# Kernel optimization log

Hardware: AMD Instinct MI355X
Metric: run time of the kernel (lower is better)

Reference implementation:

```python
import jax, jax.numpy as jnp
import numpy as np

B, D, H, W, C = 2, 16, 56, 56, 128
WD, WH, WW = 2, 7, 7
SD, SH, SW = 1, 3, 3
HEADS = 4
HEAD_DIM = C // HEADS
N = WD * WH * WW            # tokens per window = 98
NW = (D // WD) * (H // WH) * (W // WW)  # windows per batch = 512
EPS = 1e-5
SCALE = HEAD_DIM ** -0.5


def _partition_np(x):
    b, d, h, w, c = x.shape
    x = x.reshape(b, d // WD, WD, h // WH, WH, w // WW, WW, c)
    return x.transpose(0, 1, 3, 5, 2, 4, 6, 7).reshape(-1, N, c)


def _compute_attn_mask():
    # cyclic-shift mask: label 3x3x3 regions, windows mix labels -> -100
    img = np.zeros((1, D, H, W, 1), np.float32)
    cnt = 0
    for ds in (slice(0, -WD), slice(-WD, -SD), slice(-SD, None)):
        for hs in (slice(0, -WH), slice(-WH, -SH), slice(-SH, None)):
            for ws in (slice(0, -WW), slice(-WW, -SW), slice(-SW, None)):
                img[:, ds, hs, ws, :] = cnt
                cnt += 1
    mw = _partition_np(img).reshape(-1, N)          # (nW, N)
    am = mw[:, None, :] - mw[:, :, None]
    return np.where(am != 0, -100.0, 0.0).astype(np.float32)


def _rel_index():
    coords = np.stack(np.meshgrid(np.arange(WD), np.arange(WH), np.arange(WW), indexing='ij')).reshape(3, -1)
    rel = (coords[:, :, None] - coords[:, None, :]).transpose(1, 2, 0)  # (N,N,3)
    rel[..., 0] += WD - 1
    rel[..., 1] += WH - 1
    rel[..., 2] += WW - 1
    rel[..., 0] *= (2 * WH - 1) * (2 * WW - 1)
    rel[..., 1] *= 2 * WW - 1
    return rel.sum(-1).astype(np.int32)  # (N,N)


def setup_inputs() -> dict:
    key = jax.random.key(0)
    ks = jax.random.split(key, 8)
    s = 0.02
    table_size = (2 * WD - 1) * (2 * WH - 1) * (2 * WW - 1)
    return {
        'x': jax.random.normal(ks[0], (B, D, H, W, C), jnp.float32),
        'attn_mask': jnp.asarray(_compute_attn_mask()),
        'rel_index': jnp.asarray(_rel_index()),
        'norm1_g': jnp.ones((C,), jnp.float32),
        'norm1_b': jnp.zeros((C,), jnp.float32),
        'qkv_w': jax.random.normal(ks[1], (C, 3 * C), jnp.float32) * s,
        'qkv_b': jnp.zeros((3 * C,), jnp.float32),
        'rel_table': jax.random.normal(ks[2], (table_size, HEADS), jnp.float32) * s,
        'proj_w': jax.random.normal(ks[3], (C, C), jnp.float32) * s,
        'proj_b': jnp.zeros((C,), jnp.float32),
        'norm2_g': jnp.ones((C,), jnp.float32),
        'norm2_b': jnp.zeros((C,), jnp.float32),
        'fc1_w': jax.random.normal(ks[4], (C, 4 * C), jnp.float32) * s,
        'fc1_b': jnp.zeros((4 * C,), jnp.float32),
        'fc2_w': jax.random.normal(ks[5], (4 * C, C), jnp.float32) * s,
        'fc2_b': jnp.zeros((C,), jnp.float32),
    }


def _ln(x, g, b):
    mu = jnp.mean(x, -1, keepdims=True)
    var = jnp.mean(jnp.square(x - mu), -1, keepdims=True)
    return (x - mu) * jax.lax.rsqrt(var + EPS) * g + b


def _block(x, attn_mask, rel_index, norm1_g, norm1_b, qkv_w, qkv_b, rel_table,
           proj_w, proj_b, norm2_g, norm2_b, fc1_w, fc1_b, fc2_w, fc2_b):
    # ---- part1: LN -> shift -> window partition -> W-MSA -> reverse -> unshift
    h = _ln(x, norm1_g, norm1_b)
    h = jnp.roll(h, (-SD, -SH, -SW), axis=(1, 2, 3))
    # window partition -> (B*nW, N, C)
    h = h.reshape(B, D // WD, WD, H // WH, WH, W // WW, WW, C)
    h = h.transpose(0, 1, 3, 5, 2, 4, 6, 7).reshape(B * NW, N, C)
    qkv = (h @ qkv_w + qkv_b).reshape(B * NW, N, 3, HEADS, HEAD_DIM)
    qkv = qkv.transpose(2, 0, 3, 1, 4)  # (3, B_, heads, N, hd)
    q, k, v = qkv[0] * SCALE, qkv[1], qkv[2]
    attn = jnp.einsum('bhnd,bhmd->bhnm', q, k)  # (B_, heads, N, N)
    bias = rel_table[rel_index.reshape(-1)].reshape(N, N, HEADS).transpose(2, 0, 1)
    attn = attn + bias[None]
    attn = attn.reshape(B, NW, HEADS, N, N) + attn_mask[None, :, None]
    attn = jax.nn.softmax(attn.reshape(B * NW, HEADS, N, N), axis=-1)
    o = jnp.einsum('bhnm,bhmd->bhnd', attn, v)
    o = o.transpose(0, 2, 1, 3).reshape(B * NW, N, C)
    o = o @ proj_w + proj_b
    # window reverse -> (B, D, H, W, C)
    o = o.reshape(B, D // WD, H // WH, W // WW, WD, WH, WW, C)
    o = o.transpose(0, 1, 4, 2, 5, 3, 6, 7).reshape(B, D, H, W, C)
    o = jnp.roll(o, (SD, SH, SW), axis=(1, 2, 3))
    x = x + o  # drop_path = identity (rate 0)
    # ---- part2: LN -> MLP (keras gelu is exact, approximate=False)
    m = _ln(x, norm2_g, norm2_b)
    m = jax.nn.gelu(m @ fc1_w + fc1_b, approximate=False) @ fc2_w + fc2_b
    return x + m


def reference(x, attn_mask, rel_index, norm1_g, norm1_b, qkv_w, qkv_b, rel_table,
              proj_w, proj_b, norm2_g, norm2_b, fc1_w, fc1_b, fc2_w, fc2_b):
    return _block(x, attn_mask, rel_index, norm1_g, norm1_b, qkv_w, qkv_b, rel_table,
                  proj_w, proj_b, norm2_g, norm2_b, fc1_w, fc1_b, fc2_w, fc2_b)
```

## Files before the change

kernel.cpp:

```cpp
#include <hip/hip_runtime.h>
#include <math.h>

#define ROWS 100352
#define EPSL 1e-5f
#define SCALE_Q 0.17677669529663687f

typedef __attribute__((ext_vector_type(8))) short bf16x8;
typedef __attribute__((ext_vector_type(4))) float f32x4;

__device__ __forceinline__ unsigned short f2b(float f) {
  union { float f; unsigned int u; } a; a.f = f;
  unsigned int u = a.u;
  return (unsigned short)((u + 0x7FFF + ((u >> 16) & 1)) >> 16);
}

__device__ __forceinline__ int map_row(int r) {
  int t = r;
  int tw = t % 7; t /= 7;
  int th = t % 7; t /= 7;
  int td = t & 1;  t >>= 1;
  int zw = t & 7;  t >>= 3;
  int zh = t & 7;  t >>= 3;
  int zd = t & 7;  int bb = t >> 3;
  int d = zd * 2 + td;
  int h = zh * 7 + th;
  int w = zw * 7 + tw;
  int sd = (d + 1) & 15;
  int sh = h + 3; if (sh >= 56) sh -= 56;
  int sw = w + 3; if (sw >= 56) sw -= 56;
  return ((bb * 16 + sd) * 56 + sh) * 56 + sw;
}

__global__ __launch_bounds__(256) void k_prep_all(
    const float* __restrict__ qkv_w, unsigned short* __restrict__ qkvT,
    const float* __restrict__ proj_w, unsigned short* __restrict__ projT,
    const float* __restrict__ fc1_w, unsigned short* __restrict__ fc1T,
    const float* __restrict__ fc2_w, unsigned short* __restrict__ fc2T,
    const float* __restrict__ n2g)
{
  int b = blockIdx.x, tid = threadIdx.x;
  if (b < 192) {
    int id = b * 256 + tid;
    int n = id >> 7, k = id & 127;
    float v = qkv_w[(size_t)k * 384 + n];
    if (n < 128) v *= SCALE_Q;
    qkvT[id] = f2b(v);
  } else if (b < 256) {
    int id = (b - 192) * 256 + tid;
    int n = id >> 7, k = id & 127;
    projT[id] = f2b(proj_w[(size_t)k * 128 + n]);
  } else if (b < 512) {
    int id = (b - 256) * 256 + tid;
    int n = id >> 7, k = id & 127;
    fc1T[id] = f2b(fc1_w[(size_t)k * 512 + n] * n2g[k]);
  } else {
    int id = (b - 512) * 256 + tid;
    int n = id >> 9, k = id & 511;
    fc2T[id] = f2b(fc2_w[(size_t)k * 128 + n]);
  }
}

__global__ __launch_bounds__(256) void k_prep_b1(
    const float* __restrict__ fc1_b, const float* __restrict__ n2b,
    const float* __restrict__ fc1_w, float* __restrict__ b1p)
{
  int h = blockIdx.x * 256 + threadIdx.x;
  if (h >= 512) return;
  float acc = fc1_b[h];
  for (int k = 0; k < 128; ++k) acc += n2b[k] * fc1_w[(size_t)k * 512 + h];
  b1p[h] = acc;
}

__global__ __launch_bounds__(256) void k_prep_biasC(
    const int* __restrict__ relidx, const float* __restrict__ rtab,
    float* __restrict__ biasC)
{
  int id = blockIdx.x * 256 + threadIdx.x;
  int l  = id & 63;  int t = id >> 6;
  int ct = t % 7;    t /= 7;
  int rt = t & 7;    t >>= 3;
  int h  = t & 3;    int wm = t >> 2;
  int n0 = rt*16 + ((l >> 4) << 2);
  int m  = ct*16 + (l & 15);
  float4 v;
  float* vp = &v.x;
  int cm = 0;
  if (m < 98)
    cm = (m >= 49 ? 1 : 0) | ((m % 49) >= 28 ? 2 : 0) | ((m % 7) >= 4 ? 4 : 0);
  #pragma unroll
  for (int r = 0; r < 4; ++r) {
    int n = n0 + r;
    float val;
    if (m >= 98) val = -10000.f;
    else if (n >= 98) val = 0.f;
    else {
      val = rtab[relidx[n*98 + m]*4 + h];
      int cn = (n >= 49 ? 1 : 0) | ((n % 49) >= 28 ? 2 : 0) | ((n % 7) >= 4 ? 4 : 0);
      if ((cn ^ cm) & wm) val -= 100.f;
    }
    vp[r] = val;
  }
  *(float4*)(biasC + (size_t)id*4) = v;
}

__global__ __launch_bounds__(256) void k_qkv(
    const float* __restrict__ x, const float* __restrict__ g,
    const float* __restrict__ bta, const unsigned short* __restrict__ Wt,
    const float* __restrict__ bias, unsigned short* __restrict__ out)
{
  __shared__ unsigned short As[128 * 136];
  int tid = threadIdx.x;
  int row0 = blockIdx.x * 128;
  {
    int grp = tid >> 5, lane = tid & 31;
    float4 gv = *(const float4*)(g + lane*4);
    float4 bv = *(const float4*)(bta + lane*4);
    #pragma unroll
    for (int p = 0; p < 16; ++p) {
      int r = p * 8 + grp;
      size_t src = (size_t)map_row(row0 + r);
      float4 v = *(const float4*)(x + src * 128 + lane * 4);
      float s  = v.x + v.y + v.z + v.w;
      float ss = v.x*v.x + v.y*v.y + v.z*v.z + v.w*v.w;
      #pragma unroll
      for (int o = 16; o; o >>= 1) {
        s  += __shfl_xor(s,  o, 32);
        ss += __shfl_xor(ss, o, 32);
      }
      float mu   = s * (1.f/128.f);
      float rstd = rsqrtf(ss * (1.f/128.f) - mu*mu + EPSL);
      ushort4 o4;
      o4.x = f2b((v.x-mu)*rstd*gv.x + bv.x);
      o4.y = f2b((v.y-mu)*rstd*gv.y + bv.y);
      o4.z = f2b((v.z-mu)*rstd*gv.z + bv.z);
      o4.w = f2b((v.w-mu)*rstd*gv.w + bv.w);
      *(ushort4*)&As[r*136 + lane*4] = o4;
    }
  }
  __syncthreads();
  int l = tid & 63, w = tid >> 6;
  int wr = (w >> 1) * 64, wc = (w & 1) * 64;
  int fr = l & 15, gq = l >> 4, fk = gq * 8;
  for (int c = 0; c < 3; ++c) {
    int col0 = c * 128;
    float bmul = (c == 0) ? SCALE_Q : 1.f;
    f32x4 acc[4][4] = {};
    #pragma unroll
    for (int ks = 0; ks < 128; ks += 32) {
      bf16x8 af[4], bv[4];
      #pragma unroll
      for (int n = 0; n < 4; ++n)
        bv[n] = *(const bf16x8*)(Wt + (size_t)(col0 + wc + n*16 + fr)*128 + ks + fk);
      #pragma unroll
      for (int m = 0; m < 4; ++m)
        af[m] = *(bf16x8*)&As[(wr + m*16 + fr)*136 + ks + fk];
      #pragma unroll
      for (int m = 0; m < 4; ++m)
        #pragma unroll
        for (int n = 0; n < 4; ++n)
          acc[m][n] = __builtin_amdgcn_mfma_f32_16x16x32_bf16(af[m], bv[n], acc[m][n], 0, 0, 0);
    }
    #pragma unroll
    for (int m = 0; m < 4; ++m)
      #pragma unroll
      for (int r = 0; r < 4; ++r) {
        int grow = row0 + wr + m*16 + gq*4 + r;
        #pragma unroll
        for (int n = 0; n < 4; ++n) {
          int col = col0 + wc + n*16 + fr;
          out[(size_t)grow*384 + col] = f2b(acc[m][n][r] + bias[col]*bmul);
        }
      }
  }
}

__global__ __launch_bounds__(256, 4) void k_attn_mfma(
    const unsigned short* __restrict__ qkv,
    const float* __restrict__ biasC,
    unsigned short* __restrict__ o_part)
{
  __shared__ unsigned short Vt[32 * 136];
  __shared__ unsigned short Pb[128 * 120];
  int tid  = threadIdx.x;
  int bid  = blockIdx.x;
  int wg   = (bid & 7) * 512 + (bid >> 3);
  int head = wg & 3;
  int win  = wg >> 2;
  int widx = win & 511;
  int wm = ((widx >> 6) == 7 ? 1 : 0) | (((widx >> 3) & 7) == 7 ? 2 : 0)
         | ((widx & 7) == 7 ? 4 : 0);
  const unsigned short* base = qkv + (size_t)win * 98 * 384 + head * 32;

  for (int it = tid; it < 32 * 128; it += 256) {
    int d = it & 31, m = it >> 5;
    unsigned short v = 0;
    if (m < 98) v = base[m*384 + 256 + d];
    Vt[d*136 + m] = v;
  }
  for (int it = tid; it < 128 * 8; it += 256) {
    int n = it >> 3, c2 = 112 + (it & 7);
    Pb[n*120 + c2] = 0;
  }

  int l = tid & 63, w = tid >> 6;
  int fr = l & 15, g = l >> 4, fk = g * 8;
  bf16x8 zero8 = {0,0,0,0,0,0,0,0};

  bf16x8 aq[2];
  #pragma unroll
  for (int lt = 0; lt < 2; ++lt) {
    int row = (w*2 + lt)*16 + fr;
    aq[lt] = (row < 98) ? *(const bf16x8*)(base + row*384 + fk) : zero8;
  }

  const float* bcb = biasC + (size_t)(wm*4 + head) * 8 * 7 * 256;
  f32x4 S[2][7];
  #pragma unroll
  for (int ct = 0; ct < 7; ++ct) {
    int m = ct*16 + fr;
    bf16x8 kb = (m < 98) ? *(const bf16x8*)(base + m*384 + 128 + fk) : zero8;
    #pragma unroll
    for (int lt = 0; lt < 2; ++lt) {
      f32x4 bc = *(const f32x4*)(bcb + ((w*2 + lt)*7 + ct)*256 + l*4);
      S[lt][ct] = __builtin_amdgcn_mfma_f32_16x16x32_bf16(aq[lt], kb, bc, 0, 0, 0);
    }
  }

  #pragma unroll
  for (int lt = 0; lt < 2; ++lt) {
    #pragma unroll
    for (int r = 0; r < 4; ++r) {
      float mx = S[lt][0][r];
      #pragma unroll
      for (int ct = 1; ct < 7; ++ct) mx = fmaxf(mx, S[lt][ct][r]);
      #pragma unroll
      for (int o = 8; o; o >>= 1) mx = fmaxf(mx, __shfl_xor(mx, o));
      float e[7], sum = 0.f;
      #pragma unroll
      for (int ct = 0; ct < 7; ++ct) { e[ct] = __expf(S[lt][ct][r] - mx); sum += e[ct]; }
      #pragma unroll
      for (int o = 8; o; o >>= 1) sum += __shfl_xor(sum, o);
      float inv = 1.f / sum;
      #pragma unroll
      for (int ct = 0; ct < 7; ++ct) S[lt][ct][r] = e[ct] * inv;
    }
  }

  #pragma unroll
  for (int lt = 0; lt < 2; ++lt)
    #pragma unroll
    for (int ct = 0; ct < 7; ++ct) {
      int m = ct*16 + fr;
      #pragma unroll
      for (int r = 0; r < 4; ++r) {
        int n = w*32 + lt*16 + g*4 + r;
        Pb[n*120 + m] = f2b(S[lt][ct][r]);
      }
    }
  __syncthreads();

  f32x4 O[2][2] = {};
  #pragma unroll
  for (int ks = 0; ks < 4; ++ks) {
    bf16x8 ap[2], bv[2];
    #pragma unroll
    for (int lt = 0; lt < 2; ++lt) {
      int rowoff = ((w*2 + lt)*16 + fr)*120;
      if (ks < 3) ap[lt] = *(bf16x8*)&Pb[rowoff + ks*32 + fk];
      else        ap[lt] = (g < 2) ? *(bf16x8*)&Pb[rowoff + 96 + fk] : zero8;
    }
    #pragma unroll
    for (int vt = 0; vt < 2; ++vt)
      bv[vt] = *(bf16x8*)&Vt[(vt*16 + fr)*136 + ks*32 + fk];
    #pragma unroll
    for (int lt = 0; lt < 2; ++lt)
      #pragma unroll
      for (int vt = 0; vt < 2; ++vt)
        O[lt][vt] = __builtin_amdgcn_mfma_f32_16x16x32_bf16(ap[lt], bv[vt], O[lt][vt], 0, 0, 0);
  }

  #pragma unroll
  for (int lt = 0; lt < 2; ++lt)
    #pragma unroll
    for (int r = 0; r < 4; ++r) {
      int n = w*32 + lt*16 + g*4 + r;
      if (n < 98) {
        unsigned short* orow = o_part + ((size_t)win*98 + n)*128 + head*32;
        #pragma unroll
        for (int vt = 0; vt < 2; ++vt)
          orow[vt*16 + fr] = f2b(O[lt][vt][r]);
      }
    }
}

__global__ __launch_bounds__(256) void k_proj(
    const unsigned short* __restrict__ A,
    const unsigned short* __restrict__ Wt,
    const float* __restrict__ bias,
    const float* __restrict__ Xres, float* __restrict__ Cf)
{
  __shared__ unsigned short As[128 * 136];
  int tid = threadIdx.x;
  int row0 = blockIdx.x * 128;
  #pragma unroll
  for (int i = 0; i < 8; ++i) {
    int chunk = i * 256 + tid;
    int rr = chunk >> 4, off = (chunk & 15) * 8;
    *(uint4*)&As[rr*136 + off] = *(const uint4*)(A + (size_t)(row0+rr)*128 + off);
  }
  __syncthreads();
  int l = tid & 63, w = tid >> 6;
  int wr = (w >> 1) * 64, wc = (w & 1) * 64;
  int fr = l & 15, gq = l >> 4, fk = gq * 8;
  f32x4 acc[4][4] = {};
  #pragma unroll
  for (int ks = 0; ks < 128; ks += 32) {
    bf16x8 af[4], bv[4];
    #pragma unroll
    for (int n = 0; n < 4; ++n)
      bv[n] = *(const bf16x8*)(Wt + (size_t)(wc + n*16 + fr)*128 + ks + fk);
    #pragma unroll
    for (int m = 0; m < 4; ++m)
      af[m] = *(bf16x8*)&As[(wr + m*16 + fr)*136 + ks + fk];
    #pragma unroll
    for (int m = 0; m < 4; ++m)
      #pragma unroll
      for (int n = 0; n < 4; ++n)
        acc[m][n] = __builtin_amdgcn_mfma_f32_16x16x32_bf16(af[m], bv[n], acc[m][n], 0, 0, 0);
  }
  #pragma unroll
  for (int m = 0; m < 4; ++m)
    #pragma unroll
    for (int r = 0; r < 4; ++r) {
      int grow = row0 + wr + m*16 + gq*4 + r;
      size_t dst = (size_t)map_row(grow);
      #pragma unroll
      for (int n = 0; n < 4; ++n) {
        int col = wc + n*16 + fr;
        Cf[dst*128 + col] = acc[m][n][r] + bias[col] + Xres[dst*128 + col];
      }
    }
}

__global__ __launch_bounds__(256) void k_ln2(
    const float* __restrict__ x, unsigned short* __restrict__ out)
{
  int tid = threadIdx.x;
  int grp = tid >> 5, lane = tid & 31;
  size_t r = (size_t)blockIdx.x * 8 + grp;
  float4 v = *(const float4*)(x + r * 128 + lane * 4);
  float s  = v.x + v.y + v.z + v.w;
  float ss = v.x*v.x + v.y*v.y + v.z*v.z + v.w*v.w;
  #pragma unroll
  for (int o = 16; o; o >>= 1) {
    s  += __shfl_xor(s,  o, 32);
    ss += __shfl_xor(ss, o, 32);
  }
  float mu   = s * (1.f/128.f);
  float rstd = rsqrtf(ss * (1.f/128.f) - mu*mu + EPSL);
  ushort4 o4;
  o4.x = f2b((v.x-mu)*rstd);
  o4.y = f2b((v.y-mu)*rstd);
  o4.z = f2b((v.z-mu)*rstd);
  o4.w = f2b((v.w-mu)*rstd);
  *(ushort4*)(out + r*128 + lane*4) = o4;
}

__global__ __launch_bounds__(512, 4) void k_mlp(
    float* __restrict__ xio,
    const unsigned short* __restrict__ h2,
    const unsigned short* __restrict__ W1t,
    const float* __restrict__ b1p,
    const unsigned short* __restrict__ W2t,
    const float* __restrict__ b2)
{
  __shared__ unsigned short As[128 * 136];
  __shared__ unsigned short Pb[128 * 136];
  int tid = threadIdx.x;
  int row0 = blockIdx.x * 128;
  #pragma unroll
  for (int i = 0; i < 4; ++i) {
    int chunk = i * 512 + tid;
    int rr = chunk >> 4, off = (chunk & 15) * 8;
    *(uint4*)&As[rr*136 + off] = *(const uint4*)(h2 + (size_t)(row0+rr)*128 + off);
  }
  __syncthreads();
  int l = tid & 63, w = tid >> 6;
  int wr = (w & 1) * 64, wc = (w >> 1) * 32;
  int fr = l & 15, gq = l >> 4, fk = gq * 8;

  f32x4 O[4][2] = {};
  for (int j = 0; j < 4; ++j) {
    f32x4 S[4][2] = {};
    #pragma unroll
    for (int ks = 0; ks < 4; ++ks) {
      bf16x8 af[4], bv[2];
      #pragma unroll
      for (int n = 0; n < 2; ++n)
        bv[n] = *(const bf16x8*)(W1t + (size_t)(j*128 + wc + n*16 + fr)*128 + ks*32 + fk);
      #pragma unroll
      for (int m = 0; m < 4; ++m)
        af[m] = *(bf16x8*)&As[(wr + m*16 + fr)*136 + ks*32 + fk];
      #pragma unroll
      for (int m = 0; m < 4; ++m)
        #pragma unroll
        for (int n = 0; n < 2; ++n)
          S[m][n] = __builtin_amdgcn_mfma_f32_16x16x32_bf16(af[m], bv[n], S[m][n], 0, 0, 0);
    }
    #pragma unroll
    for (int m = 0; m < 4; ++m)
      #pragma unroll
      for (int n = 0; n < 2; ++n) {
        int col = wc + n*16 + fr;
        float bb = b1p[j*128 + col];
        #pragma unroll
        for (int r = 0; r < 4; ++r) {
          float v = S[m][n][r] + bb;
          float u = 1.5957691216057308f * v * (1.f + 0.044715f*v*v);
          v = v / (1.f + __expf(-u));
          Pb[(wr + m*16 + gq*4 + r)*136 + col] = f2b(v);
        }
      }
    __syncthreads();
    #pragma unroll
    for (int ks = 0; ks < 4; ++ks) {
      bf16x8 ap[4], bv[2];
      #pragma unroll
      for (int n = 0; n < 2; ++n)
        bv[n] = *(const bf16x8*)(W2t + (size_t)(wc + n*16 + fr)*512 + j*128 + ks*32 + fk);
      #pragma unroll
      for (int m = 0; m < 4; ++m)
        ap[m] = *(bf16x8*)&Pb[(wr + m*16 + fr)*136 + ks*32 + fk];
      #pragma unroll
      for (int m = 0; m < 4; ++m)
        #pragma unroll
        for (int n = 0; n < 2; ++n)
          O[m][n] = __builtin_amdgcn_mfma_f32_16x16x32_bf16(ap[m], bv[n], O[m][n], 0, 0, 0);
    }
    __syncthreads();
  }
  #pragma unroll
  for (int m = 0; m < 4; ++m)
    #pragma unroll
    for (int r = 0; r < 4; ++r) {
      size_t grow = row0 + wr + m*16 + gq*4 + r;
      #pragma unroll
      for (int n = 0; n < 2; ++n) {
        int col = wc + n*16 + fr;
        xio[grow*128 + col] += O[m][n][r] + b2[col];
      }
    }
}

extern "C" void kernel_launch(void* const* d_in, const int* in_sizes, int n_in,
                              void* d_out, int out_size, void* d_ws, size_t ws_size,
                              hipStream_t stream)
{
  const float* x         = (const float*)d_in[0];
  const int*   rel_index = (const int*)  d_in[2];
  const float* n1g       = (const float*)d_in[3];
  const float* n1b       = (const float*)d_in[4];
  const float* qkv_w     = (const float*)d_in[5];
  const float* qkv_b     = (const float*)d_in[6];
  const float* rtab      = (const float*)d_in[7];
  const float* proj_w    = (const float*)d_in[8];
  const float* proj_b    = (const float*)d_in[9];
  const float* n2g       = (const float*)d_in[10];
  const float* n2b       = (const float*)d_in[11];
  const float* fc1_w     = (const float*)d_in[12];
  const float* fc1_b     = (const float*)d_in[13];
  const float* fc2_w     = (const float*)d_in[14];
  const float* fc2_b     = (const float*)d_in[15];
  float* out = (float*)d_out;

  unsigned short* buf0  = (unsigned short*)d_ws;
  unsigned short* buf1  = buf0 + (size_t)ROWS * 384;
  unsigned short* qkvT  = buf1 + (size_t)ROWS * 128;
  unsigned short* projT = qkvT + 384 * 128;
  unsigned short* fc1T  = projT + 128 * 128;
  unsigned short* fc2T  = fc1T + 512 * 128;
  float* biasC          = (float*)(fc2T + 128 * 512);
  float* b1p            = biasC + 458752;

  k_prep_all<<<768, 256, 0, stream>>>(qkv_w, qkvT, proj_w, projT,
                                      fc1_w, fc1T, fc2_w, fc2T, n2g);
  k_prep_biasC<<<448, 256, 0, stream>>>(rel_index, rtab, biasC);
  k_prep_b1<<<2, 256, 0, stream>>>(fc1_b, n2b, fc1_w, b1p);

  k_qkv<<<ROWS/128, 256, 0, stream>>>(x, n1g, n1b, qkvT, qkv_b, buf0);

  k_attn_mfma<<<4096, 256, 0, stream>>>(buf0, biasC, buf1);

  k_proj<<<ROWS/128, 256, 0, stream>>>(buf1, projT, proj_b, x, out);

  k_ln2<<<ROWS/8, 256, 0, stream>>>(out, buf0);

  k_mlp<<<ROWS/128, 512, 0, stream>>>(out, buf0, fc1T, b1p, fc2T, fc2_b);
}
```

Before: 247.0 us.

## Fuse LayerNorm2 into proj epilogue and double-buffer MLP hidden chunks

```diff
diff --git a/kernel.cpp b/kernel.cpp
--- a/kernel.cpp
+++ b/kernel.cpp
@@ -297,9 +297,11 @@
     const unsigned short* __restrict__ A,
     const unsigned short* __restrict__ Wt,
     const float* __restrict__ bias,
-    const float* __restrict__ Xres, float* __restrict__ Cf)
+    const float* __restrict__ Xres, float* __restrict__ Cf,
+    unsigned short* __restrict__ h2out)
 {
   __shared__ unsigned short As[128 * 136];
+  __shared__ float red[128][2][2];
   int tid = threadIdx.x;
   int row0 = blockIdx.x * 128;
   #pragma unroll
@@ -328,42 +330,59 @@
       for (int n = 0; n < 4; ++n)
         acc[m][n] = __builtin_amdgcn_mfma_f32_16x16x32_bf16(af[m], bv[n], acc[m][n], 0, 0, 0);
   }
+  int dst[4][4];
   #pragma unroll
   for (int m = 0; m < 4; ++m)
     #pragma unroll
+    for (int r = 0; r < 4; ++r)
+      dst[m][r] = map_row(row0 + wr + m*16 + gq*4 + r);
+  #pragma unroll
+  for (int m = 0; m < 4; ++m)
+    #pragma unroll
+    for (int n = 0; n < 4; ++n) {
+      int col = wc + n*16 + fr;
+      float bb = bias[col];
+      #pragma unroll
+      for (int r = 0; r < 4; ++r)
+        acc[m][n][r] += bb + Xres[(size_t)dst[m][r]*128 + col];
+    }
+  #pragma unroll
+  for (int m = 0; m < 4; ++m)
+    #pragma unroll
     for (int r = 0; r < 4; ++r) {
-      int grow = row0 + wr + m*16 + gq*4 + r;
-      size_t dst = (size_t)map_row(grow);
+      float s  = acc[m][0][r] + acc[m][1][r] + acc[m][2][r] + acc[m][3][r];
+      float ss = acc[m][0][r]*acc[m][0][r] + acc[m][1][r]*acc[m][1][r]
+               + acc[m][2][r]*acc[m][2][r] + acc[m][3][r]*acc[m][3][r];
+      #pragma unroll
+      for (int o = 8; o; o >>= 1) {
+        s  += __shfl_xor(s,  o);
+        ss += __shfl_xor(ss, o);
+      }
+      if (fr == 0) {
+        int R = wr + m*16 + gq*4 + r;
+        red[R][w & 1][0] = s;
+        red[R][w & 1][1] = ss;
+      }
+    }
+  __syncthreads();
+  #pragma unroll
+  for (int m = 0; m < 4; ++m)
+    #pragma unroll
+    for (int r = 0; r < 4; ++r) {
+      int R = wr + m*16 + gq*4 + r;
+      float sum  = red[R][0][0] + red[R][1][0];
+      float ssum = red[R][0][1] + red[R][1][1];
+      float mu   = sum * (1.f/128.f);
+      float rstd = rsqrtf(ssum * (1.f/128.f) - mu*mu + EPSL);
+      size_t db = (size_t)dst[m][r] * 128;
       #pragma unroll
       for (int n = 0; n < 4; ++n) {
         int col = wc + n*16 + fr;
-        Cf[dst*128 + col] = acc[m][n][r] + bias[col] + Xres[dst*128 + col];
-      }
-    }
-}
-
-__global__ __launch_bounds__(256) void k_ln2(
-    const float* __restrict__ x, unsigned short* __restrict__ out)
-{
-  int tid = threadIdx.x;
-  int grp = tid >> 5, lane = tid & 31;
-  size_t r = (size_t)blockIdx.x * 8 + grp;
-  float4 v = *(const float4*)(x + r * 128 + lane * 4);
-  float s  = v.x + v.y + v.z + v.w;
-  float ss = v.x*v.x + v.y*v.y + v.z*v.z + v.w*v.w;
-  #pragma unroll
-  for (int o = 16; o; o >>= 1) {
-    s  += __shfl_xor(s,  o, 32);
-    ss += __shfl_xor(ss, o, 32);
-  }
-  float mu   = s * (1.f/128.f);
-  float rstd = rsqrtf(ss * (1.f/128.f) - mu*mu + EPSL);
-  ushort4 o4;
-  o4.x = f2b((v.x-mu)*rstd);
-  o4.y = f2b((v.y-mu)*rstd);
-  o4.z = f2b((v.z-mu)*rstd);
-  o4.w = f2b((v.w-mu)*rstd);
-  *(ushort4*)(out + r*128 + lane*4) = o4;
+        float t = acc[m][n][r];
+        Cf[db + col] = t;
+        h2out[db + col] = f2b((t - mu) * rstd);
+      }
+    }
 }
 
 __global__ __launch_bounds__(512, 4) void k_mlp(
@@ -375,7 +394,7 @@
     const float* __restrict__ b2)
 {
   __shared__ unsigned short As[128 * 136];
-  __shared__ unsigned short Pb[128 * 136];
+  __shared__ unsigned short Pb[2][128 * 72];
   int tid = threadIdx.x;
   int row0 = blockIdx.x * 128;
   #pragma unroll
@@ -386,51 +405,49 @@
   }
   __syncthreads();
   int l = tid & 63, w = tid >> 6;
-  int wr = (w & 1) * 64, wc = (w >> 1) * 32;
+  int wr = (w & 1) * 64, cw = w >> 1;
   int fr = l & 15, gq = l >> 4, fk = gq * 8;
+  int hl = cw * 16 + fr;
 
   f32x4 O[4][2] = {};
-  for (int j = 0; j < 4; ++j) {
-    f32x4 S[4][2] = {};
+
+  auto fc1 = [&](int jj, unsigned short* pw) {
+    f32x4 S[4] = {};
     #pragma unroll
     for (int ks = 0; ks < 4; ++ks) {
-      bf16x8 af[4], bv[2];
+      bf16x8 bv = *(const bf16x8*)(W1t + (size_t)(jj*64 + hl)*128 + ks*32 + fk);
+      #pragma unroll
+      for (int m = 0; m < 4; ++m) {
+        bf16x8 af = *(bf16x8*)&As[(wr + m*16 + fr)*136 + ks*32 + fk];
+        S[m] = __builtin_amdgcn_mfma_f32_16x16x32_bf16(af, bv, S[m], 0, 0, 0);
+      }
+    }
+    float bb = b1p[jj*64 + hl];
+    #pragma unroll
+    for (int m = 0; m < 4; ++m)
+      #pragma unroll
+      for (int r = 0; r < 4; ++r) {
+        float v = S[m][r] + bb;
+        float u = 1.5957691216057308f * v * (1.f + 0.044715f*v*v);
+        v = v / (1.f + __expf(-u));
+        pw[(wr + m*16 + gq*4 + r)*72 + hl] = f2b(v);
+      }
+  };
+
+  fc1(0, Pb[0]);
+  __syncthreads();
+  for (int j = 0; j < 8; ++j) {
+    if (j < 7) fc1(j + 1, Pb[(j + 1) & 1]);
+    const unsigned short* pb = Pb[j & 1];
+    #pragma unroll
+    for (int ks = 0; ks < 2; ++ks) {
+      bf16x8 ap[4], bv[2];
       #pragma unroll
       for (int n = 0; n < 2; ++n)
-        bv[n] = *(const bf16x8*)(W1t + (size_t)(j*128 + wc + n*16 + fr)*128 + ks*32 + fk);
+        bv[n] = *(const bf16x8*)(W2t + (size_t)(cw*32 + n*16 + fr)*512 + j*64 + ks*32 + fk);
       #pragma unroll
       for (int m = 0; m < 4; ++m)
-        af[m] = *(bf16x8*)&As[(wr + m*16 + fr)*136 + ks*32 + fk];
-      #pragma unroll
-      for (int m = 0; m < 4; ++m)
-        #pragma unroll
-        for (int n = 0; n < 2; ++n)
-          S[m][n] = __builtin_amdgcn_mfma_f32_16x16x32_bf16(af[m], bv[n], S[m][n], 0, 0, 0);
-    }
-    #pragma unroll
-    for (int m = 0; m < 4; ++m)
-      #pragma unroll
-      for (int n = 0; n < 2; ++n) {
-        int col = wc + n*16 + fr;
-        float bb = b1p[j*128 + col];
-        #pragma unroll
-        for (int r = 0; r < 4; ++r) {
-          float v = S[m][n][r] + bb;
-          float u = 1.5957691216057308f * v * (1.f + 0.044715f*v*v);
-          v = v / (1.f + __expf(-u));
-          Pb[(wr + m*16 + gq*4 + r)*136 + col] = f2b(v);
-        }
-      }
-    __syncthreads();
-    #pragma unroll
-    for (int ks = 0; ks < 4; ++ks) {
-      bf16x8 ap[4], bv[2];
-      #pragma unroll
-      for (int n = 0; n < 2; ++n)
-        bv[n] = *(const bf16x8*)(W2t + (size_t)(wc + n*16 + fr)*512 + j*128 + ks*32 + fk);
-      #pragma unroll
-      for (int m = 0; m < 4; ++m)
-        ap[m] = *(bf16x8*)&Pb[(wr + m*16 + fr)*136 + ks*32 + fk];
+        ap[m] = *(const bf16x8*)&pb[(wr + m*16 + fr)*72 + ks*32 + fk];
       #pragma unroll
       for (int m = 0; m < 4; ++m)
         #pragma unroll
@@ -446,7 +463,7 @@
       size_t grow = row0 + wr + m*16 + gq*4 + r;
       #pragma unroll
       for (int n = 0; n < 2; ++n) {
-        int col = wc + n*16 + fr;
+        int col = cw*32 + n*16 + fr;
         xio[grow*128 + col] += O[m][n][r] + b2[col];
       }
     }
@@ -491,9 +508,7 @@
 
   k_attn_mfma<<<4096, 256, 0, stream>>>(buf0, biasC, buf1);
 
-  k_proj<<<ROWS/128, 256, 0, stream>>>(buf1, projT, proj_b, x, out);
-
-  k_ln2<<<ROWS/8, 256, 0, stream>>>(out, buf0);
+  k_proj<<<ROWS/128, 256, 0, stream>>>(buf1, projT, proj_b, x, out, buf0);
 
   k_mlp<<<ROWS/128, 512, 0, stream>>>(out, buf0, fc1T, b1p, fc2T, fc2_b);
 }
```

Measured after the change: 234.6 us. -5.0%, faster.
